# Kernel optimization log

Hardware: AMD Instinct MI355X
Metric: run time of the kernel (lower is better)

## Reference

```python
import jax, jax.numpy as jnp
import numpy as np

N_FEATURES = 4096
N_GROUPS = 1024
BATCH = 8192


def _make_groups():
    # Deterministic variable-size groups: size_g = 2 + (g % 7), sizes in [2, 8].
    rng = np.random.RandomState(0)
    sizes = 2 + (np.arange(N_GROUPS) % 7)
    flat_idx = rng.randint(0, N_FEATURES, size=int(sizes.sum())).astype(np.int64)
    seg_ids = np.repeat(np.arange(N_GROUPS, dtype=np.int64), sizes)
    return flat_idx, seg_ids


def setup_inputs() -> dict:
    key = jax.random.key(0)
    k1, k2, k3, k4 = jax.random.split(key, 4)
    flat_idx_np, seg_ids_np = _make_groups()
    total = flat_idx_np.shape[0]  # 5115
    x = jax.random.normal(k1, (BATCH, N_FEATURES), dtype=jnp.float32)
    # Concatenated per-group HeNormal-style weights (shape (size,1) flattened).
    w_flat = jax.random.normal(k2, (total,), dtype=jnp.float32)
    # SimplyConnected weight (Ones init in original; random here for testing).
    diag_w = jax.random.uniform(k3, (N_GROUPS,), dtype=jnp.float32)
    # Dense kernel [n_groups, units=1], no bias.
    dense_W = jax.random.normal(k4, (N_GROUPS, 1), dtype=jnp.float32) * (2.0 / N_GROUPS) ** 0.5
    return {
        "x": x,
        "flat_idx": jnp.asarray(flat_idx_np),
        "seg_ids": jnp.asarray(seg_ids_np),
        "w_flat": w_flat,
        "diag_w": diag_w,
        "dense_W": dense_W,
    }


def reference(x, flat_idx, seg_ids, w_flat, diag_w, dense_W):
    # GroupConnected: per-group gather + (size,1) matmul == segmented weighted sum.
    # gathered: [B, total_idx]; weighted then segment-summed over groups -> [B, n_groups]
    weighted = x[:, flat_idx] * w_flat  # [B, total]
    grouped = jax.ops.segment_sum(weighted.T, seg_ids, num_segments=N_GROUPS).T  # [B, G]
    # diagblock (depth-2 = 1 SimplyConnected): elementwise scale, then Dense (no bias).
    return (grouped * diag_w) @ dense_W  # [B, units=1]
```

## Files before the change

### kernel.cpp

```cpp
#include <hip/hip_runtime.h>

#define N_FEATURES 4096
#define N_GROUPS   1024
#define BATCH      8192
#define NV4        (N_FEATURES / 4)

__global__ __launch_bounds__(1024) void build_coeff_kernel(
    const int* __restrict__ flat_idx,
    const int* __restrict__ seg_ids,
    const float* __restrict__ w_flat,
    const float* __restrict__ diag_w,
    const float* __restrict__ dense_W,
    float* __restrict__ coeff,
    int total)
{
    __shared__ float s_coeff[N_FEATURES];
    for (int i = threadIdx.x; i < N_FEATURES; i += blockDim.x) s_coeff[i] = 0.0f;
    __syncthreads();
    for (int i = threadIdx.x; i < total; i += blockDim.x) {
        int g = seg_ids[i];
        float c = w_flat[i] * diag_w[g] * dense_W[g];
        atomicAdd(&s_coeff[flat_idx[i]], c);
    }
    __syncthreads();
    for (int i = threadIdx.x; i < N_FEATURES; i += blockDim.x) coeff[i] = s_coeff[i];
}

__global__ __launch_bounds__(256, 4) void gemv_kernel(
    const float* __restrict__ x,
    const float* __restrict__ coeff,
    float* __restrict__ out)
{
    const int wid  = threadIdx.x >> 6;
    const int lane = threadIdx.x & 63;
    const int row  = (blockIdx.x << 2) + wid;

    const float4* __restrict__ xr = (const float4*)(x + (size_t)row * N_FEATURES);
    const float4* __restrict__ c4 = (const float4*)coeff;

    float4 xv[16];
#pragma unroll
    for (int k = 0; k < 16; ++k)
        xv[k] = xr[(k << 6) + lane];

    float acc = 0.0f;
#pragma unroll
    for (int k = 0; k < 16; ++k) {
        float4 cv = c4[(k << 6) + lane];
        acc += xv[k].x * cv.x + xv[k].y * cv.y + xv[k].z * cv.z + xv[k].w * cv.w;
    }

#pragma unroll
    for (int off = 32; off > 0; off >>= 1)
        acc += __shfl_down(acc, off, 64);

    if (lane == 0)
        out[row] = acc;
}

extern "C" void kernel_launch(void* const* d_in, const int* in_sizes, int n_in,
                              void* d_out, int out_size, void* d_ws, size_t ws_size,
                              hipStream_t stream) {
    const float* x        = (const float*)d_in[0];
    const int*   flat_idx = (const int*)d_in[1];
    const int*   seg_ids  = (const int*)d_in[2];
    const float* w_flat   = (const float*)d_in[3];
    const float* diag_w   = (const float*)d_in[4];
    const float* dense_W  = (const float*)d_in[5];
    float* out = (float*)d_out;
    const int total = in_sizes[1];

    float* coeff = (float*)d_ws;

    build_coeff_kernel<<<1, 1024, 0, stream>>>(flat_idx, seg_ids, w_flat,
                                               diag_w, dense_W, coeff, total);
    gemv_kernel<<<BATCH / 4, 256, 0, stream>>>(x, coeff, out);
}
```

Before: 204.5 us.

## Process four rows per wave with double-buffered x loads and register-cached coeff

Each wave in the GEMV kernel now handles four consecutive rows. It keeps the coefficient vector in registers and prefetches the next row's x values into a second register buffer while reducing the current row. The grid shrinks fourfold and launch bounds drop to two blocks per CU, so occupancy falls in exchange for more memory-level parallelism within each wave. The coefficient builder also batches its global loads into registers before running the shared-memory atomics. It assumes at most five elements per thread.

```diff
diff --git a/kernel.cpp b/kernel.cpp
--- a/kernel.cpp
+++ b/kernel.cpp
@@ -17,45 +17,80 @@
     __shared__ float s_coeff[N_FEATURES];
     for (int i = threadIdx.x; i < N_FEATURES; i += blockDim.x) s_coeff[i] = 0.0f;
     __syncthreads();
+
+    int my_idx[5]; int my_g[5]; float my_w[5];
+    int cnt = 0;
     for (int i = threadIdx.x; i < total; i += blockDim.x) {
-        int g = seg_ids[i];
-        float c = w_flat[i] * diag_w[g] * dense_W[g];
-        atomicAdd(&s_coeff[flat_idx[i]], c);
+        my_idx[cnt] = flat_idx[i];
+        my_g[cnt]   = seg_ids[i];
+        my_w[cnt]   = w_flat[i];
+        ++cnt;
+    }
+    for (int k = 0; k < cnt; ++k) {
+        float c = my_w[k] * diag_w[my_g[k]] * dense_W[my_g[k]];
+        atomicAdd(&s_coeff[my_idx[k]], c);
     }
     __syncthreads();
     for (int i = threadIdx.x; i < N_FEATURES; i += blockDim.x) coeff[i] = s_coeff[i];
 }
 
-__global__ __launch_bounds__(256, 4) void gemv_kernel(
+__global__ __launch_bounds__(256, 2) void gemv_kernel(
     const float* __restrict__ x,
     const float* __restrict__ coeff,
     float* __restrict__ out)
 {
     const int wid  = threadIdx.x >> 6;
     const int lane = threadIdx.x & 63;
-    const int row  = (blockIdx.x << 2) + wid;
+    const int wave = (blockIdx.x << 2) + wid;
+    const int row0 = wave << 2;
 
-    const float4* __restrict__ xr = (const float4*)(x + (size_t)row * N_FEATURES);
     const float4* __restrict__ c4 = (const float4*)coeff;
 
-    float4 xv[16];
+    float4 cv[16];
 #pragma unroll
     for (int k = 0; k < 16; ++k)
-        xv[k] = xr[(k << 6) + lane];
+        cv[k] = c4[(k << 6) + lane];
 
-    float acc = 0.0f;
+    const float4* __restrict__ xr = (const float4*)(x + (size_t)row0 * N_FEATURES);
+    float4 xa[16], xb[16];
 #pragma unroll
-    for (int k = 0; k < 16; ++k) {
-        float4 cv = c4[(k << 6) + lane];
-        acc += xv[k].x * cv.x + xv[k].y * cv.y + xv[k].z * cv.z + xv[k].w * cv.w;
-    }
+    for (int k = 0; k < 16; ++k)
+        xa[k] = xr[(k << 6) + lane];
 
 #pragma unroll
-    for (int off = 32; off > 0; off >>= 1)
-        acc += __shfl_down(acc, off, 64);
+    for (int r = 0; r < 4; ++r) {
+        if (r < 3) {
+            const float4* __restrict__ xn =
+                (const float4*)(x + (size_t)(row0 + r + 1) * N_FEATURES);
+            if (r & 1) {
+#pragma unroll
+                for (int k = 0; k < 16; ++k) xa[k] = xn[(k << 6) + lane];
+            } else {
+#pragma unroll
+                for (int k = 0; k < 16; ++k) xb[k] = xn[(k << 6) + lane];
+            }
+        }
 
-    if (lane == 0)
-        out[row] = acc;
+        float acc = 0.0f;
+        if (r & 1) {
+#pragma unroll
+            for (int k = 0; k < 16; ++k)
+                acc += xb[k].x * cv[k].x + xb[k].y * cv[k].y +
+                       xb[k].z * cv[k].z + xb[k].w * cv[k].w;
+        } else {
+#pragma unroll
+            for (int k = 0; k < 16; ++k)
+                acc += xa[k].x * cv[k].x + xa[k].y * cv[k].y +
+                       xa[k].z * cv[k].z + xa[k].w * cv[k].w;
+        }
+
+#pragma unroll
+        for (int off = 32; off > 0; off >>= 1)
+            acc += __shfl_down(acc, off, 64);
+
+        if (lane == 0)
+            out[row0 + r] = acc;
+    }
 }
 
 extern "C" void kernel_launch(void* const* d_in, const int* in_sizes, int n_in,
@@ -74,5 +109,5 @@
 
     build_coeff_kernel<<<1, 1024, 0, stream>>>(flat_idx, seg_ids, w_flat,
                                                diag_w, dense_W, coeff, total);
-    gemv_kernel<<<BATCH / 4, 256, 0, stream>>>(x, coeff, out);
+    gemv_kernel<<<BATCH / 16, 256, 0, stream>>>(x, coeff, out);
 }
```

Result: slower. 210.9 us (+3.1%).
